# Kernel tuning notes

Measured on AMD Instinct MI355X. Metric: run time of the kernel, lower is better.

Reference implementation:

```python
import jax, jax.numpy as jnp
import numpy as np

B, F, V, E, A = 8192, 39, 1_000_000, 16, 16  # batch, fields, vocab, embed, attn


def setup_inputs() -> dict:
    key = jax.random.key(0)
    ks = jax.random.split(key, 9)
    return {
        "feat_index": jax.random.randint(ks[0], (B, F), 0, V),
        "feat_value": jax.random.uniform(ks[1], (B, F), dtype=jnp.float32),
        "first_order_weights": jax.random.normal(ks[2], (V, 1), dtype=jnp.float32) * 0.01,
        "emb_table": jax.random.normal(ks[3], (V, E), dtype=jnp.float32) * 0.01,
        "bias": jax.random.normal(ks[4], (1,), dtype=jnp.float32),
        "attention_w": jax.random.normal(ks[5], (E, A), dtype=jnp.float32) * 0.1,
        "attention_b": jax.random.normal(ks[6], (A,), dtype=jnp.float32) * 0.1,
        "projection_h": jax.random.normal(ks[7], (A, 1), dtype=jnp.float32) * 0.1,
        "projection_p": jax.random.normal(ks[8], (E, 1), dtype=jnp.float32) * 0.1,
    }


def reference(feat_index, feat_value, first_order_weights, emb_table, bias,
              attention_w, attention_b, projection_h, projection_p):
    fv = feat_value[..., None]                                  # [B,F,1]
    # first order: gather weights, scale by value, sum over fields
    y_first = jnp.sum(first_order_weights[feat_index] * fv, axis=1)[:, 0]  # [B]
    # embeddings scaled by feature values
    emb = emb_table[feat_index] * fv                            # [B,F,E]
    # pairwise bi-interaction over all i<j field pairs (num_pairs = F*(F-1)/2)
    iu, ju = np.triu_indices(F, k=1)
    bi = emb[:, iu, :] * emb[:, ju, :]                          # [B,P,E]
    # tiny attention MLP + softmax over pairs
    att = jax.nn.relu(jnp.einsum('bpe,ea->bpa', bi, attention_w) + attention_b)
    score = jax.nn.softmax(jnp.einsum('bpa,ao->bpo', att, projection_h), axis=1)  # [B,P,1]
    pooled = jnp.sum(score * bi, axis=1)                        # [B,E]
    aw = (pooled @ projection_p)[:, 0]                          # [B]
    y = bias + y_first + aw                                     # [B]
    return jax.nn.sigmoid(y)
```

## Files before the change

### kernel.cpp

```cpp
#include <hip/hip_runtime.h>
#include <math.h>


#define BB 8192
#define FF 39
#define PP 741
#define NT 47
#define RSTR 20
#define SSTR (FF * RSTR)

typedef short bf16x8 __attribute__((ext_vector_type(8)));
typedef float f32x4  __attribute__((ext_vector_type(4)));

static __device__ __forceinline__ int pack2(float a, float b) {
    unsigned ua = __builtin_bit_cast(unsigned, a);
    unsigned ub = __builtin_bit_cast(unsigned, b);
    return (int)((ua >> 16) | (ub & 0xFFFF0000u));
}

__global__ __launch_bounds__(256)
void afm_kernel(const int*   __restrict__ fidx,
                const float* __restrict__ fval,
                const float* __restrict__ fow,
                const float* __restrict__ emb,
                const float* __restrict__ bias,
                const float* __restrict__ aw_,
                const float* __restrict__ ab_,
                const float* __restrict__ ph_,
                const float* __restrict__ pp_,
                float*       __restrict__ out)
{
    __shared__ __align__(16) float s_emb[4 * SSTR];
    __shared__ unsigned s_pij[NT * 16];

    const int tid  = threadIdx.x;
    const int wid  = tid >> 6;
    const int lane = tid & 63;
    const int c    = lane & 15;
    const int quad = lane >> 4;
    const int smp  = blockIdx.x * 4 + wid;

    if (tid < FF - 1) {
        int i = tid;
        int base = (i * (2 * FF - i - 1)) >> 1;
        for (int j = i + 1; j < FF; ++j)
            s_pij[base++] = ((unsigned)(i * 80) << 16) | (unsigned)(j * 80);
    } else if (tid == FF - 1) {
        for (int e = PP; e < NT * 16; ++e) s_pij[e] = 0u;
    }

    int ixr = 0; float vr = 0.f, fo = 0.f;
    if (lane < FF) {
        ixr = fidx[smp * FF + lane];
        vr  = fval[smp * FF + lane];
        fo  = fow[ixr] * vr;
    }
    #pragma unroll
    for (int m = 1; m < 64; m <<= 1) fo += __shfl_xor(fo, m);

    float* my = &s_emb[wid * SSTR];
    for (int u = lane; u < FF * 4; u += 64) {
        int row = u >> 2, q4 = u & 3;
        int   ix = __shfl(ixr, row);
        float v  = __shfl(vr,  row);
        const float4 ev = ((const float4*)emb)[(size_t)ix * 4 + q4];
        *(float4*)&my[row * RSTR + q4 * 4] =
            make_float4(ev.x * v, ev.y * v, ev.z * v, ev.w * v);
    }

    const f32x4 abf = ((const f32x4*)ab_)[quad];
    const f32x4 hf  = ((const f32x4*)ph_)[quad];
    bf16x8 wfrag;
    {
        float t0 = 0.f, t1 = 0.f, t2 = 0.f, t3 = 0.f,
              t4 = 0.f, t5 = 0.f, t6 = 0.f, t7 = 0.f;
        if (quad < 2) {
            const float* base = aw_ + (quad * 8) * 16 + c;
            t0 = base[0];   t1 = base[16];  t2 = base[32];  t3 = base[48];
            t4 = base[64];  t5 = base[80];  t6 = base[96];  t7 = base[112];
        }
        union { int i[4]; bf16x8 v; } u;
        u.i[0] = pack2(t0, t1); u.i[1] = pack2(t2, t3);
        u.i[2] = pack2(t4, t5); u.i[3] = pack2(t6, t7);
        wfrag = u.v;
    }

    __syncthreads();

    const char* bpre = (const char*)my + (quad & 1) * 32;
    float p0=0.f,p1=0.f,p2=0.f,p3=0.f,p4=0.f,p5=0.f,p6=0.f,p7=0.f;
    float z = 0.f;
    int pidx = c;
    for (int t = 0; t < NT; ++t, pidx += 16) {
        unsigned pk = s_pij[t * 16 + c];
        const float4* ei = (const float4*)(bpre + (pk >> 16));
        const float4* ej = (const float4*)(bpre + (pk & 0xFFFFu));
        float4 a0 = ei[0], a1 = ei[1];
        float4 b0 = ej[0], b1 = ej[1];
        float m0 = a0.x*b0.x, m1 = a0.y*b0.y, m2 = a0.z*b0.z, m3 = a0.w*b0.w;
        float m4 = a1.x*b1.x, m5 = a1.y*b1.y, m6 = a1.z*b1.z, m7 = a1.w*b1.w;
        union { int i[4]; bf16x8 v; } u;
        u.i[0] = pack2(m0, m1); u.i[1] = pack2(m2, m3);
        u.i[2] = pack2(m4, m5); u.i[3] = pack2(m6, m7);
        f32x4 acc = abf;
        acc = __builtin_amdgcn_mfma_f32_16x16x32_bf16(wfrag, u.v, acc, 0, 0, 0);
        float s = fmaf(fmaxf(acc[0], 0.f), hf[0],
                  fmaf(fmaxf(acc[1], 0.f), hf[1],
                  fmaf(fmaxf(acc[2], 0.f), hf[2],
                       fmaxf(acc[3], 0.f) * hf[3])));
        s += __shfl_xor(s, 16);
        s += __shfl_xor(s, 32);
        float w = __expf(s);
        w = (pidx < PP) ? w : 0.f;
        z += w;
        p0 = fmaf(w, m0, p0); p1 = fmaf(w, m1, p1);
        p2 = fmaf(w, m2, p2); p3 = fmaf(w, m3, p3);
        p4 = fmaf(w, m4, p4); p5 = fmaf(w, m5, p5);
        p6 = fmaf(w, m6, p6); p7 = fmaf(w, m7, p7);
    }

    const float4 pf0 = ((const float4*)pp_)[(quad & 1) * 2];
    const float4 pf1 = ((const float4*)pp_)[(quad & 1) * 2 + 1];
    float awp = fmaf(p0, pf0.x, fmaf(p1, pf0.y, fmaf(p2, pf0.z,
                fmaf(p3, pf0.w, fmaf(p4, pf1.x, fmaf(p5, pf1.y,
                fmaf(p6, pf1.z, p7 * pf1.w)))))));
    #pragma unroll
    for (int m = 1; m < 64; m <<= 1) {
        awp += __shfl_xor(awp, m);
        z   += __shfl_xor(z, m);
    }
    if (lane == 0) {
        float y = bias[0] + fo + 2.f * awp / z;
        out[smp] = 1.f / (1.f + __expf(-y));
    }
}

extern "C" void kernel_launch(void* const* d_in, const int* in_sizes, int n_in,
                              void* d_out, int out_size, void* d_ws, size_t ws_size,
                              hipStream_t stream) {
    const int*   fidx      = (const int*)  d_in[0];
    const float* fval      = (const float*)d_in[1];
    const float* fow       = (const float*)d_in[2];
    const float* emb_table = (const float*)d_in[3];
    const float* bias      = (const float*)d_in[4];
    const float* attn_w    = (const float*)d_in[5];
    const float* attn_b    = (const float*)d_in[6];
    const float* proj_h    = (const float*)d_in[7];
    const float* proj_p    = (const float*)d_in[8];
    float* out = (float*)d_out;

    afm_kernel<<<BB / 4, 256, 0, stream>>>(fidx, fval, fow, emb_table, bias,
                                           attn_w, attn_b, proj_h, proj_p, out);
}
```

Measured before the change: 143.3 us.

## Switch attention MLP to 32x32x16 MFMA covering 32 pairs per wave step

Replaces the 16x16x32 bf16 MFMA, which processed 16 pairs per iteration and duplicated work across the four quads, with a 32x32x16 MFMA that processes 32 pairs per iteration. This halves the loop trip count from 47 to 24 and removes one cross-lane shuffle per iteration. The loop is also unrolled by 4. In exchange, the larger MFMA has a longer latency and uses a 16-register accumulator, of which half the rows are padding, which raises register pressure.

```diff
diff --git a/kernel.cpp b/kernel.cpp
--- a/kernel.cpp
+++ b/kernel.cpp
@@ -5,12 +5,13 @@
 #define BB 8192
 #define FF 39
 #define PP 741
-#define NT 47
+#define NT 24
 #define RSTR 20
 #define SSTR (FF * RSTR)
 
 typedef short bf16x8 __attribute__((ext_vector_type(8)));
 typedef float f32x4  __attribute__((ext_vector_type(4)));
+typedef float f32x16 __attribute__((ext_vector_type(16)));
 
 static __device__ __forceinline__ int pack2(float a, float b) {
     unsigned ua = __builtin_bit_cast(unsigned, a);
@@ -31,13 +32,13 @@
                 float*       __restrict__ out)
 {
     __shared__ __align__(16) float s_emb[4 * SSTR];
-    __shared__ unsigned s_pij[NT * 16];
+    __shared__ unsigned s_pij[NT * 32];
 
     const int tid  = threadIdx.x;
     const int wid  = tid >> 6;
     const int lane = tid & 63;
-    const int c    = lane & 15;
-    const int quad = lane >> 4;
+    const int n    = lane & 31;
+    const int h    = lane >> 5;
     const int smp  = blockIdx.x * 4 + wid;
 
     if (tid < FF - 1) {
@@ -46,7 +47,7 @@
         for (int j = i + 1; j < FF; ++j)
             s_pij[base++] = ((unsigned)(i * 80) << 16) | (unsigned)(j * 80);
     } else if (tid == FF - 1) {
-        for (int e = PP; e < NT * 16; ++e) s_pij[e] = 0u;
+        for (int e = PP; e < NT * 32; ++e) s_pij[e] = 0u;
     }
 
     int ixr = 0; float vr = 0.f, fo = 0.f;
@@ -68,14 +69,27 @@
             make_float4(ev.x * v, ev.y * v, ev.z * v, ev.w * v);
     }
 
-    const f32x4 abf = ((const f32x4*)ab_)[quad];
-    const f32x4 hf  = ((const f32x4*)ph_)[quad];
+    const f32x4 h_lo = ((const f32x4*)ph_)[h];
+    const f32x4 h_hi = ((const f32x4*)ph_)[h + 2];
+
+    f32x16 cinit;
+    {
+        const f32x4 ab_lo = ((const f32x4*)ab_)[h];
+        const f32x4 ab_hi = ((const f32x4*)ab_)[h + 2];
+        cinit[0] = ab_lo[0]; cinit[1] = ab_lo[1];
+        cinit[2] = ab_lo[2]; cinit[3] = ab_lo[3];
+        cinit[4] = ab_hi[0]; cinit[5] = ab_hi[1];
+        cinit[6] = ab_hi[2]; cinit[7] = ab_hi[3];
+        #pragma unroll
+        for (int r = 8; r < 16; ++r) cinit[r] = 0.f;
+    }
+
     bf16x8 wfrag;
     {
         float t0 = 0.f, t1 = 0.f, t2 = 0.f, t3 = 0.f,
               t4 = 0.f, t5 = 0.f, t6 = 0.f, t7 = 0.f;
-        if (quad < 2) {
-            const float* base = aw_ + (quad * 8) * 16 + c;
+        if (n < 16) {
+            const float* base = aw_ + (8 * h) * 16 + n;
             t0 = base[0];   t1 = base[16];  t2 = base[32];  t3 = base[48];
             t4 = base[64];  t5 = base[80];  t6 = base[96];  t7 = base[112];
         }
@@ -87,12 +101,13 @@
 
     __syncthreads();
 
-    const char* bpre = (const char*)my + (quad & 1) * 32;
+    const char* bpre = (const char*)my + h * 32;
     float p0=0.f,p1=0.f,p2=0.f,p3=0.f,p4=0.f,p5=0.f,p6=0.f,p7=0.f;
     float z = 0.f;
-    int pidx = c;
-    for (int t = 0; t < NT; ++t, pidx += 16) {
-        unsigned pk = s_pij[t * 16 + c];
+    int pidx = n;
+    #pragma unroll 4
+    for (int t = 0; t < NT; ++t, pidx += 32) {
+        unsigned pk = s_pij[t * 32 + n];
         const float4* ei = (const float4*)(bpre + (pk >> 16));
         const float4* ej = (const float4*)(bpre + (pk & 0xFFFFu));
         float4 a0 = ei[0], a1 = ei[1];
@@ -102,13 +117,16 @@
         union { int i[4]; bf16x8 v; } u;
         u.i[0] = pack2(m0, m1); u.i[1] = pack2(m2, m3);
         u.i[2] = pack2(m4, m5); u.i[3] = pack2(m6, m7);
-        f32x4 acc = abf;
-        acc = __builtin_amdgcn_mfma_f32_16x16x32_bf16(wfrag, u.v, acc, 0, 0, 0);
-        float s = fmaf(fmaxf(acc[0], 0.f), hf[0],
-                  fmaf(fmaxf(acc[1], 0.f), hf[1],
-                  fmaf(fmaxf(acc[2], 0.f), hf[2],
-                       fmaxf(acc[3], 0.f) * hf[3])));
-        s += __shfl_xor(s, 16);
+        f32x16 d = __builtin_amdgcn_mfma_f32_32x32x16_bf16(wfrag, u.v, cinit,
+                                                           0, 0, 0);
+        float s = fmaf(fmaxf(d[0], 0.f), h_lo[0],
+                  fmaf(fmaxf(d[1], 0.f), h_lo[1],
+                  fmaf(fmaxf(d[2], 0.f), h_lo[2],
+                  fmaf(fmaxf(d[3], 0.f), h_lo[3],
+                  fmaf(fmaxf(d[4], 0.f), h_hi[0],
+                  fmaf(fmaxf(d[5], 0.f), h_hi[1],
+                  fmaf(fmaxf(d[6], 0.f), h_hi[2],
+                       fmaxf(d[7], 0.f) * h_hi[3])))))));
         s += __shfl_xor(s, 32);
         float w = __expf(s);
         w = (pidx < PP) ? w : 0.f;
@@ -119,8 +137,8 @@
         p6 = fmaf(w, m6, p6); p7 = fmaf(w, m7, p7);
     }
 
-    const float4 pf0 = ((const float4*)pp_)[(quad & 1) * 2];
-    const float4 pf1 = ((const float4*)pp_)[(quad & 1) * 2 + 1];
+    const float4 pf0 = ((const float4*)pp_)[2 * h];
+    const float4 pf1 = ((const float4*)pp_)[2 * h + 1];
     float awp = fmaf(p0, pf0.x, fmaf(p1, pf0.y, fmaf(p2, pf0.z,
                 fmaf(p3, pf0.w, fmaf(p4, pf1.x, fmaf(p5, pf1.y,
                 fmaf(p6, pf1.z, p7 * pf1.w)))))));
```

Result: faster. 132.6 us (-7.5%).
